# Kernel optimization log

Hardware: AMD Instinct MI355X
Metric: run time of the kernel (lower is better)

Reference implementation:

```python
import jax, jax.numpy as jnp
import numpy as np
from jax import lax

UNITS = 128
NUM_STEPS = 2048
BATCH = 32
MIN_OMEGA = 0.1
MAX_OMEGA = 70.1
DT = 1.0 / 173.61          # EEG sampling interval
INPUT_SCALER = 0.1
BETA = 0.01
TWO_PI = 2 * 3.1415        # module uses 3.1415, not math.pi


def setup_inputs() -> dict:
    key = jax.random.key(0)
    k1, k2 = jax.random.split(key)
    X_r = jax.random.normal(k1, (BATCH, NUM_STEPS, UNITS), dtype=jnp.float32)
    X_i = jax.random.normal(k2, (BATCH, NUM_STEPS, UNITS), dtype=jnp.float32)
    omegas = (jnp.linspace(MIN_OMEGA, MAX_OMEGA, UNITS) * TWO_PI).astype(jnp.float32)[None, :]  # [1, U]
    return {"X_r": X_r, "X_i": X_i, "omegas": omegas}


def reference(X_r, X_i, omegas):
    B, T, U = X_r.shape
    r0 = jnp.ones((B, U), dtype=X_r.dtype)
    phi0 = jnp.zeros((B, U), dtype=X_r.dtype)

    def step(carry, xs):
        r, phi = carry
        xr, xi = xs  # [B, U] each
        input_r = INPUT_SCALER * xr * jnp.cos(phi)
        input_phi = INPUT_SCALER * xi * jnp.sin(phi)
        r = r + ((1.0 - BETA * jnp.square(r)) * r + input_r) * DT
        phi = phi + (omegas - input_phi) * DT
        return (r, phi), (r, phi)

    xs = (jnp.transpose(X_r, (1, 0, 2)), jnp.transpose(X_i, (1, 0, 2)))  # [T, B, U]
    _, (r_seq, phi_seq) = lax.scan(step, (r0, phi0), xs)
    r = jnp.transpose(r_seq, (1, 0, 2))    # [B, T, U]
    phi = jnp.transpose(phi_seq, (1, 0, 2))
    z_real = r * jnp.cos(phi)
    z_imag = r * jnp.sin(phi)
    return (z_real, z_imag)
```

## Files before the change

kernel.cpp:

```cpp
#include <hip/hip_runtime.h>
#include <math.h>

namespace {
constexpr int kUnits = 128;
constexpr int kSteps = 2048;
constexpr int kBatch = 32;
constexpr int kSeg = 16;
constexpr int kNSeg = kSteps / kSeg;
constexpr int kUBlk = 16;
constexpr int kUPT = 2;
constexpr int kUG = kUBlk / kUPT;
constexpr int kThreads = kUG * kNSeg;
constexpr int kBlocks = kBatch * (kUnits / kUBlk);
constexpr int kGrp = 16;
constexpr int kGrpSeg = kNSeg / kGrp;
constexpr int kPad = kUBlk + 1;
constexpr double kDT = 1.0 / 173.61;
constexpr double kTwoPi = 6.283185307179586;
constexpr double kInv2Pi = 1.0 / kTwoPi;
constexpr size_t kChainElems = (size_t)kSteps * kUnits;

typedef float v2f __attribute__((ext_vector_type(2)));

struct Tables {
  float G[kSteps];
  float Gseg[kNSeg];
  float Gg[kGrp];
  float rbar0[kNSeg];
};
constexpr Tables make_tables() {
  Tables tb{};
  double r = 1.0;
  for (int t = 0; t < kSteps; ++t) {
    if (t % kSeg == 0) tb.rbar0[t / kSeg] = (float)r;
    tb.G[t] = (float)(1.0 + (1.0 - 0.03 * r * r) * kDT);
    r = r + (1.0 - 0.01 * r * r) * r * kDT;
  }
  for (int s = 0; s < kNSeg; ++s) {
    double p = 1.0;
    for (int j = 0; j < kSeg; ++j) p *= (double)tb.G[s * kSeg + j];
    tb.Gseg[s] = (float)p;
  }
  for (int g = 0; g < kGrp; ++g) {
    double p = 1.0;
    for (int s = 0; s < kGrpSeg; ++s) p *= (double)tb.Gseg[g * kGrpSeg + s];
    tb.Gg[g] = (float)p;
  }
  return tb;
}
}

__constant__ Tables kTab = make_tables();

__global__ __launch_bounds__(kThreads, 4)
void hopf_fused(const float* __restrict__ Xr, const float* __restrict__ Xi,
                const float* __restrict__ Om,
                float* __restrict__ Zr, float* __restrict__ Zi) {
  __shared__ float sG[kNSeg][kPad];
  __shared__ float sH[kNSeg][kPad];
  __shared__ float sP[kNSeg][kPad];
  __shared__ float sQ[kNSeg][kPad];
  __shared__ float cG[kGrp][kPad], cH[kGrp][kPad], cP[kGrp][kPad], cQ[kGrp][kPad];
  __shared__ float pD[kGrp][kPad], pR[kGrp][kPad];

  const int tid = threadIdx.x;
  const int ug = tid & (kUG - 1);
  const int seg = tid >> 3;
  const int b = blockIdx.x >> 3;
  const int uq = blockIdx.x & 7;
  const int u0 = uq * kUBlk + ug * kUPT;
  const int t0 = seg * kSeg;

  const size_t base = ((size_t)b * kSteps + t0) * (size_t)kUnits + u0;
  const v2f* xr2 = (const v2f*)(Xr + base);
  const v2f* xi2 = (const v2f*)(Xi + base);
  v2f xr[kSeg], xi[kSeg];
#pragma unroll
  for (int j = 0; j < kSeg; ++j) {
    xr[j] = xr2[j * (kUnits / 2)];
    xi[j] = xi2[j * (kUnits / 2)];
  }
  __builtin_amdgcn_sched_barrier(0);

  float cw[kUPT], sw[kUPT], c0[kUPT], s0[kUPT], c0i[kUPT], s0i[kUPT];
#pragma unroll
  for (int k = 0; k < kUPT; ++k) {
    const double wdt = (double)Om[u0 + k] * kDT;
    double sd, cd;
    sincos(wdt, &sd, &cd);
    cw[k] = (float)cd;
    sw[k] = (float)sd;
    const double ang = wdt * (double)t0;
    const double kk = rint(ang * kInv2Pi);
    const float th = (float)fma(-kk, kTwoPi, ang);
    __sincosf(th, &s0[k], &c0[k]);
    c0i[k] = c0[k];
    s0i[k] = s0[k];
  }

  const float cdt = (float)(0.1 * kDT);
  float gr[kUPT] = {1.f, 1.f}, hr[kUPT] = {0.f, 0.f};
  float pr[kUPT] = {0.f, 0.f}, qr[kUPT] = {0.f, 0.f};
#pragma unroll
  for (int j = 0; j < kSeg; ++j) {
    const float Ge = kTab.G[t0 + j];
#pragma unroll
    for (int k = 0; k < kUPT; ++k) {
      const float axi = cdt * xi[j][k];
      const float axr = cdt * xr[j][k];
      const float ge = fmaf(-axi, c0[k], 1.f);
      const float he = -axi * s0[k];
      const float pe = -axr * s0[k];
      const float qe = axr * c0[k];
      const float g2 = gr[k] * ge;
      const float h2 = fmaf(ge, hr[k], he);
      const float p2 = fmaf(pe, gr[k], Ge * pr[k]);
      const float q2 = fmaf(pe, hr[k], fmaf(Ge, qr[k], qe));
      gr[k] = g2; hr[k] = h2; pr[k] = p2; qr[k] = q2;
      const float c1 = fmaf(cw[k], c0[k], -(sw[k] * s0[k]));
      const float s1 = fmaf(cw[k], s0[k], sw[k] * c0[k]);
      c0[k] = c1; s0[k] = s1;
    }
  }
#pragma unroll
  for (int k = 0; k < kUPT; ++k) {
    const int ch = ug * kUPT + k;
    sG[seg][ch] = gr[k];
    sH[seg][ch] = hr[k];
    sP[seg][ch] = pr[k];
    sQ[seg][ch] = qr[k];
  }
  __syncthreads();

  if (tid < kUBlk * kGrp) {
    const int ch = tid & (kUBlk - 1);
    const int gb = tid >> 4;
    float g = 1.f, h = 0.f, p = 0.f, q = 0.f;
#pragma unroll
    for (int i = 0; i < kGrpSeg; ++i) {
      const int sg = gb * kGrpSeg + i;
      const float mg = sG[sg][ch], mh = sH[sg][ch];
      const float mp = sP[sg][ch], mq = sQ[sg][ch];
      const float Gs = kTab.Gseg[sg];
      const float g2 = mg * g;
      const float h2 = fmaf(mg, h, mh);
      const float p2 = fmaf(mp, g, Gs * p);
      const float q2 = fmaf(mp, h, fmaf(Gs, q, mq));
      g = g2; h = h2; p = p2; q = q2;
    }
    cG[gb][ch] = g; cH[gb][ch] = h; cP[gb][ch] = p; cQ[gb][ch] = q;
  }
  __syncthreads();

  if (tid < kUBlk) {
    const int ch = tid;
    float d = 0.f, rho = 0.f;
#pragma unroll
    for (int gb = 0; gb < kGrp; ++gb) {
      pD[gb][ch] = d;
      pR[gb][ch] = rho;
      const float g = cG[gb][ch], h = cH[gb][ch];
      const float p = cP[gb][ch], q = cQ[gb][ch];
      const float Gs = kTab.Gg[gb];
      const float dn = fmaf(g, d, h);
      const float rn = fmaf(p, d, fmaf(Gs, rho, q));
      d = dn; rho = rn;
    }
  }
  __syncthreads();

  if (tid < kUBlk * kGrp) {
    const int ch = tid & (kUBlk - 1);
    const int gb = tid >> 4;
    float d = pD[gb][ch], rho = pR[gb][ch];
#pragma unroll
    for (int i = 0; i < kGrpSeg; ++i) {
      const int sg = gb * kGrpSeg + i;
      const float mg = sG[sg][ch], mh = sH[sg][ch];
      const float mp = sP[sg][ch], mq = sQ[sg][ch];
      sG[sg][ch] = d;
      sH[sg][ch] = rho;
      const float Gs = kTab.Gseg[sg];
      const float dn = fmaf(mg, d, mh);
      const float rn = fmaf(mp, d, fmaf(Gs, rho, mq));
      d = dn; rho = rn;
    }
  }
  __syncthreads();

  float c[kUPT], s[kUPT], r[kUPT];
#pragma unroll
  for (int k = 0; k < kUPT; ++k) {
    const int ch = ug * kUPT + k;
    const float delta = sG[seg][ch];
    const float rho = sH[seg][ch];
    float sd, cd;
    __sincosf(delta, &sd, &cd);
    c[k] = fmaf(c0i[k], cd, -(s0i[k] * sd));
    s[k] = fmaf(s0i[k], cd, c0i[k] * sd);
    r[k] = kTab.rbar0[seg] + rho;
  }

  const float DTf = (float)kDT;
  const float nscale = -(0.1f * DTf);
  const float c01dt = 0.1f * DTf;
  v2f* zr2 = (v2f*)(Zr + base);
  v2f* zi2 = (v2f*)(Zi + base);
#pragma unroll
  for (int j = 0; j < kSeg; ++j) {
    v2f ozr, ozi;
#pragma unroll
    for (int k = 0; k < kUPT; ++k) {
      const float eps = (xi[j][k] * nscale) * s[k];
      const float A = fmaf(-sw[k], eps, cw[k]);
      const float B = fmaf(cw[k], eps, sw[k]);
      const float c2 = fmaf(A, c[k], -(B * s[k]));
      const float s2 = fmaf(A, s[k], B * c[k]);
      const float rr = r[k] * r[k];
      const float om1 = fmaf(-0.01f, rr, 1.f);
      const float racc = fmaf(xr[j][k] * c[k], c01dt, r[k]);
      r[k] = fmaf(om1 * r[k], DTf, racc);
      c[k] = c2; s[k] = s2;
      ozr[k] = r[k] * c[k];
      ozi[k] = r[k] * s[k];
    }
    __builtin_nontemporal_store(ozr, &zr2[j * (kUnits / 2)]);
    __builtin_nontemporal_store(ozi, &zi2[j * (kUnits / 2)]);
  }
}

extern "C" void kernel_launch(void* const* d_in, const int* in_sizes, int n_in,
                              void* d_out, int out_size, void* d_ws, size_t ws_size,
                              hipStream_t stream) {
  const float* Xr = (const float*)d_in[0];
  const float* Xi = (const float*)d_in[1];
  const float* Om = (const float*)d_in[2];
  float* Zr = (float*)d_out;
  float* Zi = (float*)d_out + (size_t)kBatch * kChainElems;

  hipLaunchKernelGGL(hopf_fused, dim3(kBlocks), dim3(kThreads), 0, stream,
                     Xr, Xi, Om, Zr, Zi);
}
```

Measured before the change: 123.5 us.

## Split time axis across two blocks, recomputing first-half segment summaries in second

Doubles the grid so each (batch, unit-block) pair is handled by two blocks of half the threads, each owning half the time segments. The second-half block also recomputes the segment summaries for the first half, loading its inputs directly from global memory, so it can run the full prefix scan locally without inter-block communication. This aims to raise occupancy and parallelism for the phase and radius scan. The cost is redundant reads and arithmetic for the first half of the sequence, which leaves the second-half blocks with more work than the first-half blocks.

```diff
diff --git a/kernel.cpp b/kernel.cpp
--- a/kernel.cpp
+++ b/kernel.cpp
@@ -7,11 +7,12 @@
 constexpr int kBatch = 32;
 constexpr int kSeg = 16;
 constexpr int kNSeg = kSteps / kSeg;
+constexpr int kSegB = kNSeg / 2;
 constexpr int kUBlk = 16;
 constexpr int kUPT = 2;
 constexpr int kUG = kUBlk / kUPT;
-constexpr int kThreads = kUG * kNSeg;
-constexpr int kBlocks = kBatch * (kUnits / kUBlk);
+constexpr int kThreads = kUG * kSegB;
+constexpr int kBlocks = kBatch * (kUnits / kUBlk) * 2;
 constexpr int kGrp = 16;
 constexpr int kGrpSeg = kNSeg / kGrp;
 constexpr int kPad = kUBlk + 1;
@@ -65,11 +66,15 @@
 
   const int tid = threadIdx.x;
   const int ug = tid & (kUG - 1);
-  const int seg = tid >> 3;
-  const int b = blockIdx.x >> 3;
-  const int uq = blockIdx.x & 7;
+  const int segL = tid >> 3;
+  const int bid = blockIdx.x;
+  const int half = bid >> 8;
+  const int rest = bid & 255;
+  const int b = rest >> 3;
+  const int uq = rest & 7;
   const int u0 = uq * kUBlk + ug * kUPT;
-  const int t0 = seg * kSeg;
+  const int sOwn = (half << 6) + segL;
+  const int t0 = sOwn * kSeg;
 
   const size_t base = ((size_t)b * kSteps + t0) * (size_t)kUnits + u0;
   const v2f* xr2 = (const v2f*)(Xr + base);
@@ -82,10 +87,12 @@
   }
   __builtin_amdgcn_sched_barrier(0);
 
+  double wdt_d[kUPT];
   float cw[kUPT], sw[kUPT], c0[kUPT], s0[kUPT], c0i[kUPT], s0i[kUPT];
 #pragma unroll
   for (int k = 0; k < kUPT; ++k) {
     const double wdt = (double)Om[u0 + k] * kDT;
+    wdt_d[k] = wdt;
     double sd, cd;
     sincos(wdt, &sd, &cd);
     cw[k] = (float)cd;
@@ -99,40 +106,92 @@
   }
 
   const float cdt = (float)(0.1 * kDT);
-  float gr[kUPT] = {1.f, 1.f}, hr[kUPT] = {0.f, 0.f};
-  float pr[kUPT] = {0.f, 0.f}, qr[kUPT] = {0.f, 0.f};
-#pragma unroll
-  for (int j = 0; j < kSeg; ++j) {
-    const float Ge = kTab.G[t0 + j];
+  {
+    float gr[kUPT] = {1.f, 1.f}, hr[kUPT] = {0.f, 0.f};
+    float pr[kUPT] = {0.f, 0.f}, qr[kUPT] = {0.f, 0.f};
+#pragma unroll
+    for (int j = 0; j < kSeg; ++j) {
+      const float Ge = kTab.G[t0 + j];
+#pragma unroll
+      for (int k = 0; k < kUPT; ++k) {
+        const float axi = cdt * xi[j][k];
+        const float axr = cdt * xr[j][k];
+        const float ge = fmaf(-axi, c0[k], 1.f);
+        const float he = -axi * s0[k];
+        const float pe = -axr * s0[k];
+        const float qe = axr * c0[k];
+        const float gt = gr[k] * ge;
+        const float ht = fmaf(ge, hr[k], he);
+        const float pt = fmaf(pe, gr[k], Ge * pr[k]);
+        const float qt = fmaf(pe, hr[k], fmaf(Ge, qr[k], qe));
+        gr[k] = gt; hr[k] = ht; pr[k] = pt; qr[k] = qt;
+        const float c1 = fmaf(cw[k], c0[k], -(sw[k] * s0[k]));
+        const float s1 = fmaf(cw[k], s0[k], sw[k] * c0[k]);
+        c0[k] = c1; s0[k] = s1;
+      }
+    }
 #pragma unroll
     for (int k = 0; k < kUPT; ++k) {
-      const float axi = cdt * xi[j][k];
-      const float axr = cdt * xr[j][k];
-      const float ge = fmaf(-axi, c0[k], 1.f);
-      const float he = -axi * s0[k];
-      const float pe = -axr * s0[k];
-      const float qe = axr * c0[k];
-      const float g2 = gr[k] * ge;
-      const float h2 = fmaf(ge, hr[k], he);
-      const float p2 = fmaf(pe, gr[k], Ge * pr[k]);
-      const float q2 = fmaf(pe, hr[k], fmaf(Ge, qr[k], qe));
-      gr[k] = g2; hr[k] = h2; pr[k] = p2; qr[k] = q2;
-      const float c1 = fmaf(cw[k], c0[k], -(sw[k] * s0[k]));
-      const float s1 = fmaf(cw[k], s0[k], sw[k] * c0[k]);
-      c0[k] = c1; s0[k] = s1;
-    }
-  }
-#pragma unroll
-  for (int k = 0; k < kUPT; ++k) {
-    const int ch = ug * kUPT + k;
-    sG[seg][ch] = gr[k];
-    sH[seg][ch] = hr[k];
-    sP[seg][ch] = pr[k];
-    sQ[seg][ch] = qr[k];
+      const int ch = ug * kUPT + k;
+      sG[sOwn][ch] = gr[k];
+      sH[sOwn][ch] = hr[k];
+      sP[sOwn][ch] = pr[k];
+      sQ[sOwn][ch] = qr[k];
+    }
+  }
+
+  if (half) {
+    const int t0x = segL * kSeg;
+    float cx[kUPT], sx[kUPT];
+#pragma unroll
+    for (int k = 0; k < kUPT; ++k) {
+      const double ang = wdt_d[k] * (double)t0x;
+      const double kk = rint(ang * kInv2Pi);
+      const float th = (float)fma(-kk, kTwoPi, ang);
+      __sincosf(th, &sx[k], &cx[k]);
+    }
+    const size_t basex = ((size_t)b * kSteps + t0x) * (size_t)kUnits + u0;
+    const v2f* xr2x = (const v2f*)(Xr + basex);
+    const v2f* xi2x = (const v2f*)(Xi + basex);
+    float ga[kUPT] = {1.f, 1.f}, ha[kUPT] = {0.f, 0.f};
+    float pa[kUPT] = {0.f, 0.f}, qa[kUPT] = {0.f, 0.f};
+#pragma unroll
+    for (int j = 0; j < kSeg; ++j) {
+      const v2f xrj = xr2x[j * (kUnits / 2)];
+      const v2f xij = xi2x[j * (kUnits / 2)];
+      const float Ge = kTab.G[t0x + j];
+#pragma unroll
+      for (int k = 0; k < kUPT; ++k) {
+        const float axi = cdt * xij[k];
+        const float axr = cdt * xrj[k];
+        const float ge = fmaf(-axi, cx[k], 1.f);
+        const float he = -axi * sx[k];
+        const float pe = -axr * sx[k];
+        const float qe = axr * cx[k];
+        const float gt = ga[k] * ge;
+        const float ht = fmaf(ge, ha[k], he);
+        const float pt = fmaf(pe, ga[k], Ge * pa[k]);
+        const float qt = fmaf(pe, ha[k], fmaf(Ge, qa[k], qe));
+        ga[k] = gt; ha[k] = ht; pa[k] = pt; qa[k] = qt;
+        const float c1 = fmaf(cw[k], cx[k], -(sw[k] * sx[k]));
+        const float s1 = fmaf(cw[k], sx[k], sw[k] * cx[k]);
+        cx[k] = c1; sx[k] = s1;
+      }
+    }
+#pragma unroll
+    for (int k = 0; k < kUPT; ++k) {
+      const int ch = ug * kUPT + k;
+      sG[segL][ch] = ga[k];
+      sH[segL][ch] = ha[k];
+      sP[segL][ch] = pa[k];
+      sQ[segL][ch] = qa[k];
+    }
   }
   __syncthreads();
 
-  if (tid < kUBlk * kGrp) {
+  const int nGrp = 8 << half;
+
+  if (tid < kUBlk * nGrp) {
     const int ch = tid & (kUBlk - 1);
     const int gb = tid >> 4;
     float g = 1.f, h = 0.f, p = 0.f, q = 0.f;
@@ -142,11 +201,11 @@
       const float mg = sG[sg][ch], mh = sH[sg][ch];
       const float mp = sP[sg][ch], mq = sQ[sg][ch];
       const float Gs = kTab.Gseg[sg];
-      const float g2 = mg * g;
-      const float h2 = fmaf(mg, h, mh);
-      const float p2 = fmaf(mp, g, Gs * p);
-      const float q2 = fmaf(mp, h, fmaf(Gs, q, mq));
-      g = g2; h = h2; p = p2; q = q2;
+      const float gt = mg * g;
+      const float ht = fmaf(mg, h, mh);
+      const float pt = fmaf(mp, g, Gs * p);
+      const float qt = fmaf(mp, h, fmaf(Gs, q, mq));
+      g = gt; h = ht; p = pt; q = qt;
     }
     cG[gb][ch] = g; cH[gb][ch] = h; cP[gb][ch] = p; cQ[gb][ch] = q;
   }
@@ -155,8 +214,7 @@
   if (tid < kUBlk) {
     const int ch = tid;
     float d = 0.f, rho = 0.f;
-#pragma unroll
-    for (int gb = 0; gb < kGrp; ++gb) {
+    for (int gb = 0; gb < nGrp; ++gb) {
       pD[gb][ch] = d;
       pR[gb][ch] = rho;
       const float g = cG[gb][ch], h = cH[gb][ch];
@@ -169,7 +227,7 @@
   }
   __syncthreads();
 
-  if (tid < kUBlk * kGrp) {
+  if (tid < kUBlk * nGrp) {
     const int ch = tid & (kUBlk - 1);
     const int gb = tid >> 4;
     float d = pD[gb][ch], rho = pR[gb][ch];
@@ -192,13 +250,13 @@
 #pragma unroll
   for (int k = 0; k < kUPT; ++k) {
     const int ch = ug * kUPT + k;
-    const float delta = sG[seg][ch];
-    const float rho = sH[seg][ch];
+    const float delta = sG[sOwn][ch];
+    const float rho = sH[sOwn][ch];
     float sd, cd;
     __sincosf(delta, &sd, &cd);
     c[k] = fmaf(c0i[k], cd, -(s0i[k] * sd));
     s[k] = fmaf(s0i[k], cd, c0i[k] * sd);
-    r[k] = kTab.rbar0[seg] + rho;
+    r[k] = kTab.rbar0[sOwn] + rho;
   }
 
   const float DTf = (float)kDT;
```

Measured after the change: 168.8 us. 1.37x slower.
